# Performance work log

Measured on AMD Instinct MI355X. Metric: run time of the kernel, lower is better.

The kernel has to match this reference:

```python
import jax, jax.numpy as jnp
import numpy as np

NEG = -65504.0
D = 640


def _linear(x, W, b):
    return x @ W + b


def _qkv_attention(q, k, v, mask4):
    # q:[B,Lq,D] k,v:[B,Lk,D] mask4:[B,1,1,Lk] (True = masked)
    scores = jnp.einsum('bqd,bkd->bqk', q, k) / jnp.sqrt(jnp.asarray(q.shape[-1], q.dtype))
    scores = jnp.where(mask4[:, 0, :, :], NEG, scores)  # mask.squeeze(1) -> [B,1,Lk]
    p = jax.nn.softmax(scores, axis=-1)
    return jnp.einsum('bqk,bkd->bqd', p, v)


def _attflat(x, mask4, W1, b1, W2, b2, Wm, bm):
    # x:[B,N,D]; glimpses == 1
    att = _linear(jax.nn.relu(_linear(x, W1, b1)), W2, b2)  # [B,N,1]
    m = mask4[:, 0, 0, :, None]                              # [B,N,1]
    att = jnp.where(m, NEG, att)
    att = jax.nn.softmax(att, axis=1)
    pooled = jnp.sum(att * x, axis=1)                        # [B,D]
    return _linear(pooled, Wm, bm), att[..., 0]              # att.squeeze() -> [B,N]


def setup_inputs() -> dict:
    key = jax.random.key(0)
    ks = jax.random.split(key, 16)
    B, Ni, Nq = 64, 512, 128
    s = 0.02
    inp = {
        'i_batch': jax.random.normal(ks[0], (B, Ni, D), jnp.float32),
        'q_batch': jax.random.normal(ks[1], (B, Nq, D), jnp.float32),
        'i_mask': jax.random.bernoulli(ks[2], 0.3, (B, 1, 1, Ni)),
        'q_mask': jax.random.bernoulli(ks[3], 0.3, (B, 1, 1, Nq)),
        # l_flatten params (applied to image-side features)
        'lW1': jax.random.normal(ks[4], (D, 2 * D), jnp.float32) * s,
        'lb1': jnp.zeros((2 * D,), jnp.float32),
        'lW2': jax.random.normal(ks[5], (2 * D, 1), jnp.float32) * s,
        'lb2': jnp.zeros((1,), jnp.float32),
        'lWm': jax.random.normal(ks[6], (D, D), jnp.float32) * s,
        'lbm': jnp.zeros((D,), jnp.float32),
        # i_flatten params (applied to language-side features)
        'iW1': jax.random.normal(ks[7], (D, 2 * D), jnp.float32) * s,
        'ib1': jnp.zeros((2 * D,), jnp.float32),
        'iW2': jax.random.normal(ks[8], (2 * D, 1), jnp.float32) * s,
        'ib2': jnp.zeros((1,), jnp.float32),
        'iWm': jax.random.normal(ks[9], (D, D), jnp.float32) * s,
        'ibm': jnp.zeros((D,), jnp.float32),
    }
    return inp


def reference(i_batch, q_batch, i_mask, q_mask,
              lW1, lb1, lW2, lb2, lWm, lbm,
              iW1, ib1, iW2, ib2, iWm, ibm):
    # image attends over question tokens
    i_feat = _qkv_attention(i_batch, q_batch, q_batch, q_mask)   # [B,Ni,D]
    i_feat, i_weight = _attflat(i_feat, i_mask, lW1, lb1, lW2, lb2, lWm, lbm)
    # question attends over image regions
    l_feat = _qkv_attention(q_batch, i_batch, i_batch, i_mask)   # [B,Nq,D]
    l_feat, _ = _attflat(l_feat, q_mask, iW1, ib1, iW2, ib2, iWm, ibm)
    return (i_feat, l_feat, i_weight)
```

## Files before the change

### kernel.cpp

```cpp
#include <hip/hip_runtime.h>
#include <cstdint>

#define DEV __device__ __forceinline__

typedef __attribute__((ext_vector_type(8))) short bf16x8;
typedef __attribute__((ext_vector_type(4))) float f32x4;

static constexpr int B  = 64;
static constexpr int NI = 512;
static constexpr int NQ = 128;
static constexpr int D  = 640;
static constexpr int H  = 1280;
static constexpr float NEGV  = -65504.0f;
static constexpr float SCALE = 0.039528470752104745f;

DEV unsigned short f2bf(float f) {
  union { float f; uint32_t u; } c; c.f = f;
  uint32_t u = c.u;
  u += 0x7fffu + ((u >> 16) & 1u);
  return (unsigned short)(u >> 16);
}
DEV float bf2f(unsigned short h) {
  union { uint32_t u; float f; } c; c.u = ((uint32_t)h) << 16;
  return c.f;
}

DEV void gll16(const void* g, void* l) {
  __builtin_amdgcn_global_load_lds(
      (const __attribute__((address_space(1))) void*)(uintptr_t)g,
      (__attribute__((address_space(3))) void*)(uint32_t)(uintptr_t)l,
      16, 0, 0);
}

DEV void stage64(const unsigned short* src, int ld, unsigned short* lds, int tid) {
  const int w = tid >> 6, lane = tid & 63;
#pragma unroll
  for (int i = 0; i < 4; ++i) {
    int c = w * 256 + i * 64 + lane;
    int r = c >> 3, ck = c & 7;
    int col8 = ((ck ^ (r & 7)) << 3);
    gll16(src + (long)r * ld + col8, (char*)lds + (size_t)c * 16);
  }
}

DEV bf16x8 frag(const unsigned short* ls, int row, int q) {
  return *(const bf16x8*)&ls[row * 64 + (((q ^ (row & 7))) << 3)];
}

template<int OUT_BF16>
__global__ __launch_bounds__(256, 2) void gemm_nt(
    const unsigned short* __restrict__ A, const unsigned short* __restrict__ Bt,
    void* __restrict__ C, int lda, int ldb, int ldc, int K,
    long sA, long sB, long sC)
{
  __shared__ __align__(16) unsigned short lsA[128 * 64];
  __shared__ __align__(16) unsigned short lsB[128 * 64];
  const int tid = threadIdx.x;
  const int w = tid >> 6, lane = tid & 63;
  const int wm = w >> 1, wn = w & 1;
  const int g = lane >> 4, r = lane & 15;
  const long zb = blockIdx.z;
  const unsigned short* Ab = A + zb * sA + (long)blockIdx.x * 128 * lda;
  const unsigned short* Bb = Bt + zb * sB + (long)blockIdx.y * 128 * ldb;

  f32x4 acc[4][4] = {};
  for (int k0 = 0; k0 < K; k0 += 64) {
    stage64(Ab + k0, lda, lsA, tid);
    stage64(Bb + k0, ldb, lsB, tid);
    __syncthreads();
#pragma unroll
    for (int kk = 0; kk < 2; ++kk) {
      bf16x8 af[4], bfr[4];
#pragma unroll
      for (int mi = 0; mi < 4; ++mi) af[mi]  = frag(lsA, wm * 64 + mi * 16 + r, kk * 4 + g);
#pragma unroll
      for (int ni = 0; ni < 4; ++ni) bfr[ni] = frag(lsB, wn * 64 + ni * 16 + r, kk * 4 + g);
#pragma unroll
      for (int mi = 0; mi < 4; ++mi)
#pragma unroll
        for (int ni = 0; ni < 4; ++ni)
          acc[mi][ni] = __builtin_amdgcn_mfma_f32_16x16x32_bf16(af[mi], bfr[ni], acc[mi][ni], 0, 0, 0);
    }
    __syncthreads();
  }
  const int row0 = blockIdx.x * 128 + wm * 64;
  const int col0 = blockIdx.y * 128 + wn * 64;
#pragma unroll
  for (int mi = 0; mi < 4; ++mi)
#pragma unroll
    for (int ni = 0; ni < 4; ++ni)
#pragma unroll
      for (int j = 0; j < 4; ++j) {
        int rr = row0 + mi * 16 + g * 4 + j;
        int cc = col0 + ni * 16 + r;
        float v = acc[mi][ni][j];
        if (OUT_BF16)
          ((unsigned short*)C)[zb * sC + (long)rr * ldc + cc] = f2bf(v);
        else
          ((float*)C)[zb * sC + (long)rr * ldc + cc] = v;
      }
}

__global__ __launch_bounds__(256, 2) void hatt_k(
    const unsigned short* __restrict__ A, const unsigned short* __restrict__ Bt,
    const float* __restrict__ b1, const float* __restrict__ W2,
    float* __restrict__ outlogit)
{
  __shared__ __align__(16) unsigned short lsA[128 * 64];
  __shared__ __align__(16) unsigned short lsB[128 * 64];
  __shared__ float b1c[128], w2c[128];
  const int tid = threadIdx.x;
  const int w = tid >> 6, lane = tid & 63;
  const int wm = w >> 1, wn = w & 1;
  const int g = lane >> 4, r = lane & 15;
  const int n0 = blockIdx.x * 128;
  const int m0 = blockIdx.y * 128;
  if (tid < 128) { b1c[tid] = b1[n0 + tid]; w2c[tid] = W2[n0 + tid]; }
  const unsigned short* Ab = A + (long)m0 * D;
  const unsigned short* Bb = Bt + (long)n0 * D;

  f32x4 acc[4][4] = {};
  for (int k0 = 0; k0 < D; k0 += 64) {
    stage64(Ab + k0, D, lsA, tid);
    stage64(Bb + k0, D, lsB, tid);
    __syncthreads();
#pragma unroll
    for (int kk = 0; kk < 2; ++kk) {
      bf16x8 af[4], bfr[4];
#pragma unroll
      for (int mi = 0; mi < 4; ++mi) af[mi]  = frag(lsA, wm * 64 + mi * 16 + r, kk * 4 + g);
#pragma unroll
      for (int ni = 0; ni < 4; ++ni) bfr[ni] = frag(lsB, wn * 64 + ni * 16 + r, kk * 4 + g);
#pragma unroll
      for (int mi = 0; mi < 4; ++mi)
#pragma unroll
        for (int ni = 0; ni < 4; ++ni)
          acc[mi][ni] = __builtin_amdgcn_mfma_f32_16x16x32_bf16(af[mi], bfr[ni], acc[mi][ni], 0, 0, 0);
    }
    __syncthreads();
  }
  float rs[4][4];
#pragma unroll
  for (int mi = 0; mi < 4; ++mi)
#pragma unroll
    for (int j = 0; j < 4; ++j) rs[mi][j] = 0.f;
#pragma unroll
  for (int mi = 0; mi < 4; ++mi)
#pragma unroll
    for (int ni = 0; ni < 4; ++ni)
#pragma unroll
      for (int j = 0; j < 4; ++j) {
        int cl = wn * 64 + ni * 16 + r;
        float h = acc[mi][ni][j] + b1c[cl];
        h = fmaxf(h, 0.f);
        rs[mi][j] += h * w2c[cl];
      }
#pragma unroll
  for (int mi = 0; mi < 4; ++mi)
#pragma unroll
    for (int j = 0; j < 4; ++j) {
      float v = rs[mi][j];
      v += __shfl_xor(v, 1); v += __shfl_xor(v, 2);
      v += __shfl_xor(v, 4); v += __shfl_xor(v, 8);
      if (r == 0) atomicAdd(&outlogit[m0 + wm * 64 + mi * 16 + g * 4 + j], v);
    }
}

template<int L>
__global__ void sm_scores(const float* __restrict__ S, const int* __restrict__ mask,
                          unsigned short* __restrict__ P, int M)
{
  constexpr int NV = L / 64;
  const int wid = threadIdx.x >> 6, lane = threadIdx.x & 63;
  const long row = (long)blockIdx.x * 4 + wid;
  const int b = (int)(row / M);
  const float* s = S + row * (long)L;
  const int* mk = mask + (long)b * L;
  float x[NV];
  float mx = -__builtin_inff();
#pragma unroll
  for (int i = 0; i < NV; ++i) {
    int idx = i * 64 + lane;
    float v = s[idx] * SCALE;
    x[i] = mk[idx] ? NEGV : v;
    mx = fmaxf(mx, x[i]);
  }
#pragma unroll
  for (int sft = 32; sft >= 1; sft >>= 1) mx = fmaxf(mx, __shfl_xor(mx, sft));
  float sum = 0.f;
#pragma unroll
  for (int i = 0; i < NV; ++i) { x[i] = __expf(x[i] - mx); sum += x[i]; }
#pragma unroll
  for (int sft = 32; sft >= 1; sft >>= 1) sum += __shfl_xor(sum, sft);
  const float inv = 1.f / sum;
  unsigned short* p = P + row * (long)L;
#pragma unroll
  for (int i = 0; i < NV; ++i) p[i * 64 + lane] = f2bf(x[i] * inv);
}

template<int L>
__global__ void sm_att(const float* __restrict__ logit, const int* __restrict__ mask,
                       const float* __restrict__ b2p, float* __restrict__ att,
                       float* __restrict__ iw)
{
  constexpr int PER = (L + 255) / 256;
  __shared__ float red[4];
  const int tid = threadIdx.x, b = blockIdx.x;
  const float b2v = b2p[0];
  float xs[PER];
  float mx = -__builtin_inff();
#pragma unroll
  for (int i = 0; i < PER; ++i) {
    int idx = tid + i * 256;
    if (idx < L) {
      float v = mask[(long)b * L + idx] ? NEGV : (logit[(long)b * L + idx] + b2v);
      xs[i] = v; mx = fmaxf(mx, v);
    } else xs[i] = -__builtin_inff();
  }
#pragma unroll
  for (int s = 32; s >= 1; s >>= 1) mx = fmaxf(mx, __shfl_xor(mx, s));
  if ((tid & 63) == 0) red[tid >> 6] = mx;
  __syncthreads();
  mx = fmaxf(fmaxf(red[0], red[1]), fmaxf(red[2], red[3]));
  __syncthreads();
  float sum = 0.f;
#pragma unroll
  for (int i = 0; i < PER; ++i) {
    int idx = tid + i * 256;
    if (idx < L) { xs[i] = __expf(xs[i] - mx); sum += xs[i]; }
  }
#pragma unroll
  for (int s = 32; s >= 1; s >>= 1) sum += __shfl_xor(sum, s);
  if ((tid & 63) == 0) red[tid >> 6] = sum;
  __syncthreads();
  sum = red[0] + red[1] + red[2] + red[3];
  const float inv = 1.f / sum;
#pragma unroll
  for (int i = 0; i < PER; ++i) {
    int idx = tid + i * 256;
    if (idx < L) {
      float a = xs[i] * inv;
      att[(long)b * L + idx] = a;
      if (iw) iw[(long)b * L + idx] = a;
    }
  }
}

template<int L>
__global__ void pooled_k(const float* __restrict__ att, const unsigned short* __restrict__ X,
                         float* __restrict__ out)
{
  __shared__ float a[L];
  __shared__ float part[4][64];
  const int b = blockIdx.x, tid = threadIdx.x;
  const int dcol = tid & 63, grp = tid >> 6;
  const int d = blockIdx.y * 64 + dcol;
  for (int i = tid; i < L; i += 256) a[i] = att[(long)b * L + i];
  __syncthreads();
  const unsigned short* xb = X + (long)b * L * D + d;
  float acc = 0.f;
  const int m0 = grp * (L / 4);
#pragma unroll 4
  for (int m = m0; m < m0 + L / 4; ++m) acc += a[m] * bf2f(xb[(long)m * D]);
  part[grp][dcol] = acc;
  __syncthreads();
  if (tid < 64)
    out[b * D + blockIdx.y * 64 + tid] = part[0][tid] + part[1][tid] + part[2][tid] + part[3][tid];
}

__global__ void final_k(const float* __restrict__ pooled, const float* __restrict__ W,
                        const float* __restrict__ bias, float* __restrict__ out)
{
  __shared__ float p[160];
  const int b = blockIdx.x, tid = threadIdx.x;
  const int nn = blockIdx.y * 128 + tid;
  const int k0 = blockIdx.z * 160;
  for (int i = tid; i < 160; i += 128) p[i] = pooled[b * D + k0 + i];
  __syncthreads();
  float acc = (blockIdx.z == 0) ? bias[nn] : 0.f;
  for (int k = 0; k < 160; ++k) acc += p[k] * W[(long)(k0 + k) * D + nn];
  atomicAdd(&out[b * D + nn], acc);
}

__global__ void cast_t_k(const float* __restrict__ in, unsigned short* __restrict__ outN,
                         unsigned short* __restrict__ outT, int R, int C)
{
  __shared__ float t[32][33];
  const int tx = threadIdx.x, ty = threadIdx.y;
  const long base = (long)blockIdx.z * R * C;
  const float* ib = in + base;
  unsigned short* obN = outN + base;
  unsigned short* obT = outT + base;
  const int c0 = blockIdx.x * 32, r0 = blockIdx.y * 32;
#pragma unroll
  for (int k = 0; k < 4; ++k) {
    float v = ib[(long)(r0 + ty + k * 8) * C + c0 + tx];
    t[ty + k * 8][tx] = v;
    obN[(long)(r0 + ty + k * 8) * C + c0 + tx] = f2bf(v);
  }
  __syncthreads();
#pragma unroll
  for (int k = 0; k < 4; ++k)
    obT[(long)(c0 + ty + k * 8) * R + r0 + tx] = f2bf(t[tx][ty + k * 8]);
}

__global__ void tcast_k(const float* __restrict__ in, unsigned short* __restrict__ out, int R, int C)
{
  __shared__ float t[32][33];
  const int tx = threadIdx.x, ty = threadIdx.y;
  const float* ib = in;
  unsigned short* ob = out;
  const int c0 = blockIdx.x * 32, r0 = blockIdx.y * 32;
#pragma unroll
  for (int k = 0; k < 4; ++k)
    t[ty + k * 8][tx] = ib[(long)(r0 + ty + k * 8) * C + c0 + tx];
  __syncthreads();
#pragma unroll
  for (int k = 0; k < 4; ++k)
    ob[(long)(c0 + ty + k * 8) * R + r0 + tx] = f2bf(t[tx][ty + k * 8]);
}

extern "C" void kernel_launch(void* const* d_in, const int* in_sizes, int n_in,
                              void* d_out, int out_size, void* d_ws, size_t ws_size,
                              hipStream_t stream)
{
  (void)in_sizes; (void)n_in; (void)out_size; (void)ws_size;
  const float* i_batch = (const float*)d_in[0];
  const float* q_batch = (const float*)d_in[1];
  const int*   i_mask  = (const int*)d_in[2];
  const int*   q_mask  = (const int*)d_in[3];
  const float* lW1 = (const float*)d_in[4];
  const float* lb1 = (const float*)d_in[5];
  const float* lW2 = (const float*)d_in[6];
  const float* lb2 = (const float*)d_in[7];
  const float* lWm = (const float*)d_in[8];
  const float* lbm = (const float*)d_in[9];
  const float* iW1 = (const float*)d_in[10];
  const float* ib1 = (const float*)d_in[11];
  const float* iW2 = (const float*)d_in[12];
  const float* ib2 = (const float*)d_in[13];
  const float* iWm = (const float*)d_in[14];
  const float* ibm = (const float*)d_in[15];
  float* out_if = (float*)d_out;
  float* out_lf = out_if + B * D;
  float* out_iw = out_lf + B * D;

  char* wp = (char*)d_ws;
  size_t off = 0;
  auto alloc = [&](size_t bytes) { void* p = wp + off; off += (bytes + 255) & ~(size_t)255; return p; };
  unsigned short* i_bf   = (unsigned short*)alloc((size_t)B * NI * D * 2);
  unsigned short* i_bfT  = (unsigned short*)alloc((size_t)B * NI * D * 2);
  unsigned short* q_bf   = (unsigned short*)alloc((size_t)B * NQ * D * 2);
  unsigned short* q_bfT  = (unsigned short*)alloc((size_t)B * NQ * D * 2);
  unsigned short* x1_bf  = (unsigned short*)alloc((size_t)B * NI * D * 2);
  unsigned short* x2_bf  = (unsigned short*)alloc((size_t)B * NQ * D * 2);
  float*          scores = (float*)alloc((size_t)B * NI * NQ * 4);
  unsigned short* p_bf   = (unsigned short*)alloc((size_t)B * NI * NQ * 2);
  unsigned short* lW1t   = (unsigned short*)alloc((size_t)H * D * 2);
  unsigned short* iW1t   = (unsigned short*)alloc((size_t)H * D * 2);
  float* logit1  = (float*)alloc((size_t)B * NI * 4);
  float* att1    = (float*)alloc((size_t)B * NI * 4);
  float* logit2  = (float*)alloc((size_t)B * NQ * 4);
  float* att2    = (float*)alloc((size_t)B * NQ * 4);
  float* pooled1 = (float*)alloc((size_t)B * D * 4);
  float* pooled2 = (float*)alloc((size_t)B * D * 4);

  hipMemsetAsync(out_if, 0, (size_t)2 * B * D * 4, stream);
  hipMemsetAsync(logit1, 0, (size_t)B * NI * 4, stream);
  hipMemsetAsync(logit2, 0, (size_t)B * NQ * 4, stream);

  cast_t_k<<<dim3(D / 32, NI / 32, B), dim3(32, 8), 0, stream>>>(i_batch, i_bf, i_bfT, NI, D);
  cast_t_k<<<dim3(D / 32, NQ / 32, B), dim3(32, 8), 0, stream>>>(q_batch, q_bf, q_bfT, NQ, D);
  tcast_k<<<dim3(H / 32, D / 32), dim3(32, 8), 0, stream>>>(lW1, lW1t, D, H);
  tcast_k<<<dim3(H / 32, D / 32), dim3(32, 8), 0, stream>>>(iW1, iW1t, D, H);

  gemm_nt<0><<<dim3(NI / 128, NQ / 128, B), 256, 0, stream>>>(
      i_bf, q_bf, scores, D, D, NQ, D, (long)NI * D, (long)NQ * D, (long)NI * NQ);
  sm_scores<NQ><<<dim3(B * NI / 4), 256, 0, stream>>>(scores, q_mask, p_bf, NI);
  gemm_nt<1><<<dim3(NI / 128, D / 128, B), 256, 0, stream>>>(
      p_bf, q_bfT, x1_bf, NQ, NQ, D, NQ, (long)NI * NQ, (long)D * NQ, (long)NI * D);
  hatt_k<<<dim3(H / 128, B * NI / 128), 256, 0, stream>>>(x1_bf, lW1t, lb1, lW2, logit1);
  sm_att<NI><<<dim3(B), 256, 0, stream>>>(logit1, i_mask, lb2, att1, out_iw);
  pooled_k<NI><<<dim3(B, D / 64), 256, 0, stream>>>(att1, x1_bf, pooled1);
  final_k<<<dim3(B, D / 128, 4), 128, 0, stream>>>(pooled1, lWm, lbm, out_if);

  gemm_nt<0><<<dim3(NQ / 128, NI / 128, B), 256, 0, stream>>>(
      q_bf, i_bf, scores, D, D, NI, D, (long)NQ * D, (long)NI * D, (long)NQ * NI);
  sm_scores<NI><<<dim3(B * NQ / 4), 256, 0, stream>>>(scores, i_mask, p_bf, NQ);
  gemm_nt<1><<<dim3(NQ / 128, D / 128, B), 256, 0, stream>>>(
      p_bf, i_bfT, x2_bf, NI, NI, D, NI, (long)NQ * NI, (long)D * NI, (long)NQ * D);
  hatt_k<<<dim3(H / 128, B * NQ / 128), 256, 0, stream>>>(x2_bf, iW1t, ib1, iW2, logit2);
  sm_att<NQ><<<dim3(B), 256, 0, stream>>>(logit2, q_mask, ib2, att2, nullptr);
  pooled_k<NQ><<<dim3(B, D / 64), 256, 0, stream>>>(att2, x2_bf, pooled2);
  final_k<<<dim3(B, D / 128, 4), 128, 0, stream>>>(pooled2, iWm, ibm, out_lf);
}
```

Measured before the change: 434.0 us.

## Fuse QK+softmax, add XCD swizzle, vectorize casts and pooling, raise occupancy

Adds a fused QK^T + masked softmax kernel for the image-side attention, so the fp32 scores round trip and the separate softmax launch go away. GEMM and hidden-attention grids are flattened and remapped with an XCD-aware block swizzle, and their launch bounds are raised to 4 blocks per CU. The cast/transpose kernels are merged into a templated 64x64 tile version with float4 loads, and pooling now uses 512 threads with paired bf16 loads. The memsets are combined into one call. The fused kernel uses 64KB of LDS per block, which limits occupancy, and the higher launch bounds may cause register spills.

```diff
diff --git a/kernel.cpp b/kernel.cpp
--- a/kernel.cpp
+++ b/kernel.cpp
@@ -25,6 +25,10 @@
   return c.f;
 }
 
+DEV int xcd_swz(int bid, int nwg) {
+  return (bid & 7) * (nwg >> 3) + (bid >> 3);
+}
+
 DEV void gll16(const void* g, void* l) {
   __builtin_amdgcn_global_load_lds(
       (const __attribute__((address_space(1))) void*)(uintptr_t)g,
@@ -48,10 +52,10 @@
 }
 
 template<int OUT_BF16>
-__global__ __launch_bounds__(256, 2) void gemm_nt(
+__global__ __launch_bounds__(256, 4) void gemm_nt(
     const unsigned short* __restrict__ A, const unsigned short* __restrict__ Bt,
     void* __restrict__ C, int lda, int ldb, int ldc, int K,
-    long sA, long sB, long sC)
+    long sA, long sB, long sC, int gx, int gy)
 {
   __shared__ __align__(16) unsigned short lsA[128 * 64];
   __shared__ __align__(16) unsigned short lsB[128 * 64];
@@ -59,9 +63,14 @@
   const int w = tid >> 6, lane = tid & 63;
   const int wm = w >> 1, wn = w & 1;
   const int g = lane >> 4, r = lane & 15;
-  const long zb = blockIdx.z;
-  const unsigned short* Ab = A + zb * sA + (long)blockIdx.x * 128 * lda;
-  const unsigned short* Bb = Bt + zb * sB + (long)blockIdx.y * 128 * ldb;
+  const int wg = xcd_swz(blockIdx.x, gridDim.x);
+  const int bz = wg / (gx * gy);
+  const int r2 = wg - bz * gx * gy;
+  const int by = r2 / gx;
+  const int bx = r2 - by * gx;
+  const long zb = bz;
+  const unsigned short* Ab = A + zb * sA + (long)bx * 128 * lda;
+  const unsigned short* Bb = Bt + zb * sB + (long)by * 128 * ldb;
 
   f32x4 acc[4][4] = {};
   for (int k0 = 0; k0 < K; k0 += 64) {
@@ -83,8 +92,8 @@
     }
     __syncthreads();
   }
-  const int row0 = blockIdx.x * 128 + wm * 64;
-  const int col0 = blockIdx.y * 128 + wn * 64;
+  const int row0 = bx * 128 + wm * 64;
+  const int col0 = by * 128 + wn * 64;
 #pragma unroll
   for (int mi = 0; mi < 4; ++mi)
 #pragma unroll
@@ -101,11 +110,80 @@
       }
 }
 
-__global__ __launch_bounds__(256, 2) void hatt_k(
+__global__ __launch_bounds__(256, 2) void qksm_k(
+    const unsigned short* __restrict__ A, const unsigned short* __restrict__ Bt,
+    const int* __restrict__ mask, unsigned short* __restrict__ P)
+{
+  __shared__ __align__(16) float S[128 * 128];
+  unsigned short* lsA = (unsigned short*)S;
+  unsigned short* lsB = lsA + 128 * 64;
+  const int tid = threadIdx.x;
+  const int w = tid >> 6, lane = tid & 63;
+  const int wm = w >> 1, wn = w & 1;
+  const int g = lane >> 4, r = lane & 15;
+  const int wg = xcd_swz(blockIdx.x, gridDim.x);
+  const int mt = wg & 3, b = wg >> 2;
+  const unsigned short* Ab = A + ((long)b * NI + (long)mt * 128) * D;
+  const unsigned short* Bb = Bt + (long)b * NQ * D;
+
+  f32x4 acc[4][4] = {};
+  for (int k0 = 0; k0 < D; k0 += 64) {
+    stage64(Ab + k0, D, lsA, tid);
+    stage64(Bb + k0, D, lsB, tid);
+    __syncthreads();
+#pragma unroll
+    for (int kk = 0; kk < 2; ++kk) {
+      bf16x8 af[4], bfr[4];
+#pragma unroll
+      for (int mi = 0; mi < 4; ++mi) af[mi]  = frag(lsA, wm * 64 + mi * 16 + r, kk * 4 + g);
+#pragma unroll
+      for (int ni = 0; ni < 4; ++ni) bfr[ni] = frag(lsB, wn * 64 + ni * 16 + r, kk * 4 + g);
+#pragma unroll
+      for (int mi = 0; mi < 4; ++mi)
+#pragma unroll
+        for (int ni = 0; ni < 4; ++ni)
+          acc[mi][ni] = __builtin_amdgcn_mfma_f32_16x16x32_bf16(af[mi], bfr[ni], acc[mi][ni], 0, 0, 0);
+    }
+    __syncthreads();
+  }
+#pragma unroll
+  for (int mi = 0; mi < 4; ++mi)
+#pragma unroll
+    for (int ni = 0; ni < 4; ++ni)
+#pragma unroll
+      for (int j = 0; j < 4; ++j) {
+        int rr = wm * 64 + mi * 16 + g * 4 + j;
+        int cc = wn * 64 + ni * 16 + r;
+        S[rr * 128 + (cc ^ ((rr & 7) << 2))] = acc[mi][ni][j] * SCALE;
+      }
+  __syncthreads();
+  const int* mk = mask + (long)b * NQ;
+  const int mk0 = mk[lane], mk1 = mk[lane + 64];
+  for (int t = 0; t < 32; ++t) {
+    const int rr = w * 32 + t;
+    const int off = (rr & 7) << 2;
+    float x0 = mk0 ? NEGV : S[rr * 128 + (lane ^ off)];
+    float x1 = mk1 ? NEGV : S[rr * 128 + ((lane + 64) ^ off)];
+    float mx = fmaxf(x0, x1);
+#pragma unroll
+    for (int s = 32; s >= 1; s >>= 1) mx = fmaxf(mx, __shfl_xor(mx, s));
+    float e0 = __expf(x0 - mx), e1 = __expf(x1 - mx);
+    float sum = e0 + e1;
+#pragma unroll
+    for (int s = 32; s >= 1; s >>= 1) sum += __shfl_xor(sum, s);
+    const float inv = 1.f / sum;
+    unsigned short* pr = P + ((long)b * NI + (long)mt * 128 + rr) * NQ;
+    pr[lane] = f2bf(e0 * inv);
+    pr[lane + 64] = f2bf(e1 * inv);
+  }
+}
+
+__global__ __launch_bounds__(256, 4) void hatt_k(
     const unsigned short* __restrict__ A, const unsigned short* __restrict__ Bt,
     const float* __restrict__ b1, const float* __restrict__ W2,
     float* __restrict__ outlogit)
 {
+  constexpr int NH = H / 128;
   __shared__ __align__(16) unsigned short lsA[128 * 64];
   __shared__ __align__(16) unsigned short lsB[128 * 64];
   __shared__ float b1c[128], w2c[128];
@@ -113,8 +191,9 @@
   const int w = tid >> 6, lane = tid & 63;
   const int wm = w >> 1, wn = w & 1;
   const int g = lane >> 4, r = lane & 15;
-  const int n0 = blockIdx.x * 128;
-  const int m0 = blockIdx.y * 128;
+  const int wg = xcd_swz(blockIdx.x, gridDim.x);
+  const int n0 = (wg % NH) * 128;
+  const int m0 = (wg / NH) * 128;
   if (tid < 128) { b1c[tid] = b1[n0 + tid]; w2c[tid] = W2[n0 + tid]; }
   const unsigned short* Ab = A + (long)m0 * D;
   const unsigned short* Bb = Bt + (long)n0 * D;
@@ -251,21 +330,29 @@
                          float* __restrict__ out)
 {
   __shared__ float a[L];
-  __shared__ float part[4][64];
+  __shared__ float2 part[8][64];
   const int b = blockIdx.x, tid = threadIdx.x;
-  const int dcol = tid & 63, grp = tid >> 6;
-  const int d = blockIdx.y * 64 + dcol;
-  for (int i = tid; i < L; i += 256) a[i] = att[(long)b * L + i];
-  __syncthreads();
-  const unsigned short* xb = X + (long)b * L * D + d;
-  float acc = 0.f;
-  const int m0 = grp * (L / 4);
+  const int lane = tid & 63, grp = tid >> 6;
+  const int d0 = blockIdx.y * 128 + lane * 2;
+  for (int i = tid; i < L; i += 512) a[i] = att[(long)b * L + i];
+  __syncthreads();
+  const unsigned short* xb = X + (long)b * L * D + d0;
+  float s0 = 0.f, s1 = 0.f;
+  const int m0 = grp * (L / 8);
 #pragma unroll 4
-  for (int m = m0; m < m0 + L / 4; ++m) acc += a[m] * bf2f(xb[(long)m * D]);
-  part[grp][dcol] = acc;
-  __syncthreads();
-  if (tid < 64)
-    out[b * D + blockIdx.y * 64 + tid] = part[0][tid] + part[1][tid] + part[2][tid] + part[3][tid];
+  for (int m = m0; m < m0 + L / 8; ++m) {
+    ushort2 v = *(const ushort2*)&xb[(long)m * D];
+    float av = a[m];
+    s0 += av * bf2f(v.x); s1 += av * bf2f(v.y);
+  }
+  part[grp][lane] = make_float2(s0, s1);
+  __syncthreads();
+  if (tid < 64) {
+    float r0 = 0.f, r1 = 0.f;
+#pragma unroll
+    for (int gi = 0; gi < 8; ++gi) { r0 += part[gi][tid].x; r1 += part[gi][tid].y; }
+    *(float2*)&out[b * D + blockIdx.y * 128 + tid * 2] = make_float2(r0, r1);
+  }
 }
 
 __global__ void final_k(const float* __restrict__ pooled, const float* __restrict__ W,
@@ -282,42 +369,37 @@
   atomicAdd(&out[b * D + nn], acc);
 }
 
+template<int WRITE_N>
 __global__ void cast_t_k(const float* __restrict__ in, unsigned short* __restrict__ outN,
                          unsigned short* __restrict__ outT, int R, int C)
 {
-  __shared__ float t[32][33];
-  const int tx = threadIdx.x, ty = threadIdx.y;
+  __shared__ float t[64][65];
+  const int tid = threadIdx.x;
+  const int cg = tid & 15, rw = tid >> 4;
   const long base = (long)blockIdx.z * R * C;
-  const float* ib = in + base;
-  unsigned short* obN = outN + base;
-  unsigned short* obT = outT + base;
-  const int c0 = blockIdx.x * 32, r0 = blockIdx.y * 32;
-#pragma unroll
-  for (int k = 0; k < 4; ++k) {
-    float v = ib[(long)(r0 + ty + k * 8) * C + c0 + tx];
-    t[ty + k * 8][tx] = v;
-    obN[(long)(r0 + ty + k * 8) * C + c0 + tx] = f2bf(v);
-  }
-  __syncthreads();
-#pragma unroll
-  for (int k = 0; k < 4; ++k)
-    obT[(long)(c0 + ty + k * 8) * R + r0 + tx] = f2bf(t[tx][ty + k * 8]);
-}
-
-__global__ void tcast_k(const float* __restrict__ in, unsigned short* __restrict__ out, int R, int C)
-{
-  __shared__ float t[32][33];
-  const int tx = threadIdx.x, ty = threadIdx.y;
-  const float* ib = in;
-  unsigned short* ob = out;
-  const int c0 = blockIdx.x * 32, r0 = blockIdx.y * 32;
-#pragma unroll
-  for (int k = 0; k < 4; ++k)
-    t[ty + k * 8][tx] = ib[(long)(r0 + ty + k * 8) * C + c0 + tx];
-  __syncthreads();
-#pragma unroll
-  for (int k = 0; k < 4; ++k)
-    ob[(long)(c0 + ty + k * 8) * R + r0 + tx] = f2bf(t[tx][ty + k * 8]);
+  const int c0 = blockIdx.x * 64, r0 = blockIdx.y * 64;
+#pragma unroll
+  for (int p = 0; p < 4; ++p) {
+    int row = p * 16 + rw;
+    float4 v = *(const float4*)&in[base + (long)(r0 + row) * C + c0 + cg * 4];
+    *(float4*)&t[row][cg * 4] = v;
+    if (WRITE_N) {
+      ushort4 o;
+      o.x = f2bf(v.x); o.y = f2bf(v.y); o.z = f2bf(v.z); o.w = f2bf(v.w);
+      *(ushort4*)&outN[base + (long)(r0 + row) * C + c0 + cg * 4] = o;
+    }
+  }
+  __syncthreads();
+#pragma unroll
+  for (int p = 0; p < 4; ++p) {
+    int ocol = p * 16 + rw;
+    ushort4 o;
+    o.x = f2bf(t[cg * 4 + 0][ocol]);
+    o.y = f2bf(t[cg * 4 + 1][ocol]);
+    o.z = f2bf(t[cg * 4 + 2][ocol]);
+    o.w = f2bf(t[cg * 4 + 3][ocol]);
+    *(ushort4*)&outT[base + (long)(c0 + ocol) * R + r0 + cg * 4] = o;
+  }
 }
 
 extern "C" void kernel_launch(void* const* d_in, const int* in_sizes, int n_in,
@@ -354,7 +436,7 @@
   unsigned short* q_bfT  = (unsigned short*)alloc((size_t)B * NQ * D * 2);
   unsigned short* x1_bf  = (unsigned short*)alloc((size_t)B * NI * D * 2);
   unsigned short* x2_bf  = (unsigned short*)alloc((size_t)B * NQ * D * 2);
-  float*          scores = (float*)alloc((size_t)B * NI * NQ * 4);
+  float*          scores = (float*)alloc((size_t)B * NQ * NI * 4);
   unsigned short* p_bf   = (unsigned short*)alloc((size_t)B * NI * NQ * 2);
   unsigned short* lW1t   = (unsigned short*)alloc((size_t)H * D * 2);
   unsigned short* iW1t   = (unsigned short*)alloc((size_t)H * D * 2);
@@ -366,31 +448,31 @@
   float* pooled2 = (float*)alloc((size_t)B * D * 4);
 
   hipMemsetAsync(out_if, 0, (size_t)2 * B * D * 4, stream);
-  hipMemsetAsync(logit1, 0, (size_t)B * NI * 4, stream);
-  hipMemsetAsync(logit2, 0, (size_t)B * NQ * 4, stream);
-
-  cast_t_k<<<dim3(D / 32, NI / 32, B), dim3(32, 8), 0, stream>>>(i_batch, i_bf, i_bfT, NI, D);
-  cast_t_k<<<dim3(D / 32, NQ / 32, B), dim3(32, 8), 0, stream>>>(q_batch, q_bf, q_bfT, NQ, D);
-  tcast_k<<<dim3(H / 32, D / 32), dim3(32, 8), 0, stream>>>(lW1, lW1t, D, H);
-  tcast_k<<<dim3(H / 32, D / 32), dim3(32, 8), 0, stream>>>(iW1, iW1t, D, H);
-
-  gemm_nt<0><<<dim3(NI / 128, NQ / 128, B), 256, 0, stream>>>(
-      i_bf, q_bf, scores, D, D, NQ, D, (long)NI * D, (long)NQ * D, (long)NI * NQ);
-  sm_scores<NQ><<<dim3(B * NI / 4), 256, 0, stream>>>(scores, q_mask, p_bf, NI);
-  gemm_nt<1><<<dim3(NI / 128, D / 128, B), 256, 0, stream>>>(
-      p_bf, q_bfT, x1_bf, NQ, NQ, D, NQ, (long)NI * NQ, (long)D * NQ, (long)NI * D);
-  hatt_k<<<dim3(H / 128, B * NI / 128), 256, 0, stream>>>(x1_bf, lW1t, lb1, lW2, logit1);
+  hipMemsetAsync(logit1, 0, (size_t)(B * NI * 2 + B * NQ * 2) * 4, stream);
+
+  cast_t_k<1><<<dim3(D / 64, NI / 64, B), 256, 0, stream>>>(i_batch, i_bf, i_bfT, NI, D);
+  cast_t_k<1><<<dim3(D / 64, NQ / 64, B), 256, 0, stream>>>(q_batch, q_bf, q_bfT, NQ, D);
+  cast_t_k<0><<<dim3(H / 64, D / 64, 1), 256, 0, stream>>>(lW1, nullptr, lW1t, D, H);
+  cast_t_k<0><<<dim3(H / 64, D / 64, 1), 256, 0, stream>>>(iW1, nullptr, iW1t, D, H);
+
+  qksm_k<<<dim3(4 * B), 256, 0, stream>>>(i_bf, q_bf, q_mask, p_bf);
+  gemm_nt<1><<<dim3((NI / 128) * (D / 128) * B), 256, 0, stream>>>(
+      p_bf, q_bfT, x1_bf, NQ, NQ, D, NQ, (long)NI * NQ, (long)D * NQ, (long)NI * D,
+      NI / 128, D / 128);
+  hatt_k<<<dim3((H / 128) * (B * NI / 128)), 256, 0, stream>>>(x1_bf, lW1t, lb1, lW2, logit1);
   sm_att<NI><<<dim3(B), 256, 0, stream>>>(logit1, i_mask, lb2, att1, out_iw);
-  pooled_k<NI><<<dim3(B, D / 64), 256, 0, stream>>>(att1, x1_bf, pooled1);
+  pooled_k<NI><<<dim3(B, D / 128), 512, 0, stream>>>(att1, x1_bf, pooled1);
   final_k<<<dim3(B, D / 128, 4), 128, 0, stream>>>(pooled1, lWm, lbm, out_if);
 
-  gemm_nt<0><<<dim3(NQ / 128, NI / 128, B), 256, 0, stream>>>(
-      q_bf, i_bf, scores, D, D, NI, D, (long)NQ * D, (long)NI * D, (long)NQ * NI);
+  gemm_nt<0><<<dim3((NQ / 128) * (NI / 128) * B), 256, 0, stream>>>(
+      q_bf, i_bf, scores, D, D, NI, D, (long)NQ * D, (long)NI * D, (long)NQ * NI,
+      NQ / 128, NI / 128);
   sm_scores<NI><<<dim3(B * NQ / 4), 256, 0, stream>>>(scores, i_mask, p_bf, NQ);
-  gemm_nt<1><<<dim3(NQ / 128, D / 128, B), 256, 0, stream>>>(
-      p_bf, i_bfT, x2_bf, NI, NI, D, NI, (long)NQ * NI, (long)D * NI, (long)NQ * D);
-  hatt_k<<<dim3(H / 128, B * NQ / 128), 256, 0, stream>>>(x2_bf, iW1t, ib1, iW2, logit2);
+  gemm_nt<1><<<dim3((NQ / 128) * (D / 128) * B), 256, 0, stream>>>(
+      p_bf, i_bfT, x2_bf, NI, NI, D, NI, (long)NQ * NI, (long)D * NI, (long)NQ * D,
+      NQ / 128, D / 128);
+  hatt_k<<<dim3((H / 128) * (B * NQ / 128)), 256, 0, stream>>>(x2_bf, iW1t, ib1, iW2, logit2);
   sm_att<NQ><<<dim3(B), 256, 0, stream>>>(logit2, q_mask, ib2, att2, nullptr);
-  pooled_k<NQ><<<dim3(B, D / 64), 256, 0, stream>>>(att2, x2_bf, pooled2);
+  pooled_k<NQ><<<dim3(B, D / 128), 512, 0, stream>>>(att2, x2_bf, pooled2);
   final_k<<<dim3(B, D / 128, 4), 128, 0, stream>>>(pooled2, iWm, ibm, out_lf);
 }
```

Result: no change. 427.8 us (-1.4%).
